# Kernel optimization log

Hardware: AMD Instinct MI355X
Metric: run time of the kernel (lower is better)

The kernel has to match this reference:

```python
import jax, jax.numpy as jnp
import numpy as np

T, H, I = 8192, 2048, 768  # tokens, hidden_size, intermediate_size

def setup_inputs() -> dict:
    key = jax.random.key(0)
    k1, k2, k3, k4 = jax.random.split(key, 4)
    x = jax.random.normal(k1, (T, H), dtype=jnp.float32)
    # torch nn.Linear weight layout: [out_features, in_features]
    gate_w = jax.random.normal(k2, (I, H), dtype=jnp.float32) * (1.0 / np.sqrt(H))
    up_w = jax.random.normal(k3, (I, H), dtype=jnp.float32) * (1.0 / np.sqrt(H))
    down_w = jax.random.normal(k4, (H, I), dtype=jnp.float32) * (1.0 / np.sqrt(I))
    return {"x": x, "gate_w": gate_w, "up_w": up_w, "down_w": down_w}

def reference(x, gate_w, up_w, down_w):
    # fused SwiGLU MLP: down( silu(x @ gate^T) * (x @ up^T) )
    gate = jnp.einsum('th,ih->ti', x, gate_w)   # [T, I]
    up = jnp.einsum('th,ih->ti', x, up_w)       # [T, I]
    h = jax.nn.silu(gate) * up                   # [T, I]
    out = jnp.einsum('ti,hi->th', h, down_w)     # [T, H]
    return out
```

## Files before the change

kernel.cpp:

```cpp
#include <hip/hip_runtime.h>
#include <hip/hip_bf16.h>
#include <stdint.h>

#define T_DIM 8192
#define H_DIM 2048
#define I_DIM 768

typedef __bf16 bf16_t;
typedef bf16_t bf16x8 __attribute__((ext_vector_type(8)));
typedef bf16_t bf16x4 __attribute__((ext_vector_type(4)));
typedef float  f32x4  __attribute__((ext_vector_type(4)));

__device__ __forceinline__ void async_load16(const void* g, void* s) {
    __builtin_amdgcn_global_load_lds(
        (const __attribute__((address_space(1))) void*)g,
        (__attribute__((address_space(3))) void*)s, 16, 0, 0);
}

__global__ __launch_bounds__(256) void cvt_kernel(
    const float* __restrict__ X, const float* __restrict__ G,
    const float* __restrict__ U, const float* __restrict__ D,
    bf16_t* __restrict__ Xb, bf16_t* __restrict__ Gb,
    bf16_t* __restrict__ Ub, bf16_t* __restrict__ Db)
{
    const size_t N4X = (size_t)T_DIM * H_DIM / 4;
    const size_t N4W = (size_t)I_DIM * H_DIM / 4;
    const size_t total = N4X + 3 * N4W;
    for (size_t i = (size_t)blockIdx.x * blockDim.x + threadIdx.x; i < total;
         i += (size_t)gridDim.x * blockDim.x) {
        const float* s; bf16_t* d; size_t j = i;
        if (j < N4X) { s = X; d = Xb; }
        else {
            j -= N4X;
            if (j < N4W) { s = G; d = Gb; }
            else { j -= N4W;
                if (j < N4W) { s = U; d = Ub; }
                else { j -= N4W; s = D; d = Db; } }
        }
        float4 v = ((const float4*)s)[j];
        bf16x4 o;
        o[0] = (bf16_t)v.x; o[1] = (bf16_t)v.y; o[2] = (bf16_t)v.z; o[3] = (bf16_t)v.w;
        ((bf16x4*)d)[j] = o;
    }
}

__global__ __launch_bounds__(256) void gateup_kernel(
    const bf16_t* __restrict__ X,
    const bf16_t* __restrict__ Wg,
    const bf16_t* __restrict__ Wu,
    bf16_t* __restrict__ Hbuf)
{
    __shared__ __align__(16) bf16_t sA[128 * 32];
    __shared__ __align__(16) bf16_t sG[64 * 32];
    __shared__ __align__(16) bf16_t sU[64 * 32];

    const int tid   = threadIdx.x;
    const int lane  = tid & 63;
    const int wave  = tid >> 6;
    const int waveM = wave >> 1;
    const int waveN = wave & 1;
    const int quad  = lane >> 4;
    const int lrow  = lane & 15;

    const int blockM = blockIdx.x;
    const int blockN = blockIdx.y;

    f32x4 accG[4][2], accU[4][2];
#pragma unroll
    for (int i = 0; i < 4; i++)
#pragma unroll
        for (int j = 0; j < 2; j++) { accG[i][j] = (f32x4)(0.f); accU[i][j] = (f32x4)(0.f); }

    const int s0 = tid, s1 = tid + 256;
    const int rA0 = s0 >> 2, cA0 = (s0 & 3) * 8;
    const int rA1 = s1 >> 2, cA1 = (s1 & 3) * 8;
    const int rW  = tid >> 2, cW  = (tid & 3) * 8;

    const bf16_t* Ab = X  + (size_t)(blockM * 128) * H_DIM;
    const bf16_t* Gb = Wg + (size_t)(blockN * 64) * H_DIM;
    const bf16_t* Ub = Wu + (size_t)(blockN * 64) * H_DIM;

    for (int k0 = 0; k0 < H_DIM; k0 += 32) {
        async_load16(Ab + (size_t)rA0 * H_DIM + k0 + cA0, &sA[s0 * 8]);
        async_load16(Ab + (size_t)rA1 * H_DIM + k0 + cA1, &sA[s1 * 8]);
        async_load16(Gb + (size_t)rW  * H_DIM + k0 + cW,  &sG[tid * 8]);
        async_load16(Ub + (size_t)rW  * H_DIM + k0 + cW,  &sU[tid * 8]);
        __syncthreads();

        bf16x8 aF[4], gF[2], uF[2];
#pragma unroll
        for (int mi = 0; mi < 4; mi++) {
            int r = waveM * 64 + mi * 16 + lrow;
            aF[mi] = *(const bf16x8*)&sA[r * 32 + quad * 8];
        }
#pragma unroll
        for (int ni = 0; ni < 2; ni++) {
            int r = waveN * 32 + ni * 16 + lrow;
            gF[ni] = *(const bf16x8*)&sG[r * 32 + quad * 8];
            uF[ni] = *(const bf16x8*)&sU[r * 32 + quad * 8];
        }
        __syncthreads();

#pragma unroll
        for (int mi = 0; mi < 4; mi++)
#pragma unroll
            for (int ni = 0; ni < 2; ni++) {
                accG[mi][ni] = __builtin_amdgcn_mfma_f32_16x16x32_bf16(aF[mi], gF[ni], accG[mi][ni], 0, 0, 0);
                accU[mi][ni] = __builtin_amdgcn_mfma_f32_16x16x32_bf16(aF[mi], uF[ni], accU[mi][ni], 0, 0, 0);
            }
    }

#pragma unroll
    for (int mi = 0; mi < 4; mi++) {
#pragma unroll
        for (int ni = 0; ni < 2; ni++) {
#pragma unroll
            for (int r = 0; r < 4; r++) {
                int row = blockM * 128 + waveM * 64 + mi * 16 + quad * 4 + r;
                int col = blockN * 64 + waveN * 32 + ni * 16 + lrow;
                float g = accG[mi][ni][r];
                float u = accU[mi][ni][r];
                float h = (g / (1.f + __expf(-g))) * u;
                Hbuf[(size_t)row * I_DIM + col] = (bf16_t)h;
            }
        }
    }
}

__global__ __launch_bounds__(256) void down_kernel(
    const bf16_t* __restrict__ Hbuf,
    const bf16_t* __restrict__ Wd,
    float* __restrict__ Out)
{
    __shared__ __align__(16) bf16_t sA[128 * 32];
    __shared__ __align__(16) bf16_t sB[128 * 32];

    const int tid   = threadIdx.x;
    const int lane  = tid & 63;
    const int wave  = tid >> 6;
    const int waveM = wave >> 1;
    const int waveN = wave & 1;
    const int quad  = lane >> 4;
    const int lrow  = lane & 15;

    const int blockM = blockIdx.x;
    const int blockN = blockIdx.y;

    f32x4 acc[4][4];
#pragma unroll
    for (int i = 0; i < 4; i++)
#pragma unroll
        for (int j = 0; j < 4; j++) acc[i][j] = (f32x4)(0.f);

    const int s0 = tid, s1 = tid + 256;
    const int rA0 = s0 >> 2, cA0 = (s0 & 3) * 8;
    const int rA1 = s1 >> 2, cA1 = (s1 & 3) * 8;

    const bf16_t* Ab = Hbuf + (size_t)(blockM * 128) * I_DIM;
    const bf16_t* Bb = Wd   + (size_t)(blockN * 128) * I_DIM;

    for (int k0 = 0; k0 < I_DIM; k0 += 32) {
        async_load16(Ab + (size_t)rA0 * I_DIM + k0 + cA0, &sA[s0 * 8]);
        async_load16(Ab + (size_t)rA1 * I_DIM + k0 + cA1, &sA[s1 * 8]);
        async_load16(Bb + (size_t)rA0 * I_DIM + k0 + cA0, &sB[s0 * 8]);
        async_load16(Bb + (size_t)rA1 * I_DIM + k0 + cA1, &sB[s1 * 8]);
        __syncthreads();

        bf16x8 aF[4], bF[4];
#pragma unroll
        for (int mi = 0; mi < 4; mi++) {
            int r = waveM * 64 + mi * 16 + lrow;
            aF[mi] = *(const bf16x8*)&sA[r * 32 + quad * 8];
        }
#pragma unroll
        for (int ni = 0; ni < 4; ni++) {
            int r = waveN * 64 + ni * 16 + lrow;
            bF[ni] = *(const bf16x8*)&sB[r * 32 + quad * 8];
        }
        __syncthreads();

#pragma unroll
        for (int mi = 0; mi < 4; mi++)
#pragma unroll
            for (int ni = 0; ni < 4; ni++)
                acc[mi][ni] = __builtin_amdgcn_mfma_f32_16x16x32_bf16(aF[mi], bF[ni], acc[mi][ni], 0, 0, 0);
    }

#pragma unroll
    for (int mi = 0; mi < 4; mi++) {
#pragma unroll
        for (int ni = 0; ni < 4; ni++) {
#pragma unroll
            for (int r = 0; r < 4; r++) {
                int row = blockM * 128 + waveM * 64 + mi * 16 + quad * 4 + r;
                int col = blockN * 128 + waveN * 64 + ni * 16 + lrow;
                Out[(size_t)row * H_DIM + col] = acc[mi][ni][r];
            }
        }
    }
}

extern "C" void kernel_launch(void* const* d_in, const int* in_sizes, int n_in,
                              void* d_out, int out_size, void* d_ws, size_t ws_size,
                              hipStream_t stream) {
    const float* x  = (const float*)d_in[0];
    const float* gw = (const float*)d_in[1];
    const float* uw = (const float*)d_in[2];
    const float* dw = (const float*)d_in[3];
    float* out = (float*)d_out;

    bf16_t* xb = (bf16_t*)d_ws;
    bf16_t* gb = xb + (size_t)T_DIM * H_DIM;
    bf16_t* ub = gb + (size_t)I_DIM * H_DIM;
    bf16_t* db = ub + (size_t)I_DIM * H_DIM;
    bf16_t* hb = db + (size_t)I_DIM * H_DIM;

    cvt_kernel<<<2048, 256, 0, stream>>>(x, gw, uw, dw, xb, gb, ub, db);
    gateup_kernel<<<dim3(T_DIM / 128, I_DIM / 64), 256, 0, stream>>>(xb, gb, ub, hb);
    down_kernel<<<dim3(T_DIM / 128, H_DIM / 128), 256, 0, stream>>>(hb, db, out);
}
```

Baseline: 229.2 us.

## Fuse activation bf16 conversion into gate/up GEMM and shrink down-proj tile

Stops converting x to bf16 in a separate pass. The gate/up kernel now loads fp32 x directly, converts it in registers and writes it to shared memory, while the weights keep using async LDS loads. The weight-only conversion kernel uses 8-wide vectors with one element group per thread. The down-projection N tile shrinks from 128 to 64, doubling the grid. This removes a full read and write of x through a bf16 copy, but x loads become synchronous register loads per K step, and every block re-converts its tile of x.

```diff
diff --git a/kernel.cpp b/kernel.cpp
--- a/kernel.cpp
+++ b/kernel.cpp
@@ -8,7 +8,6 @@
 
 typedef __bf16 bf16_t;
 typedef bf16_t bf16x8 __attribute__((ext_vector_type(8)));
-typedef bf16_t bf16x4 __attribute__((ext_vector_type(4)));
 typedef float  f32x4  __attribute__((ext_vector_type(4)));
 
 __device__ __forceinline__ void async_load16(const void* g, void* s) {
@@ -17,35 +16,27 @@
         (__attribute__((address_space(3))) void*)s, 16, 0, 0);
 }
 
-__global__ __launch_bounds__(256) void cvt_kernel(
-    const float* __restrict__ X, const float* __restrict__ G,
-    const float* __restrict__ U, const float* __restrict__ D,
-    bf16_t* __restrict__ Xb, bf16_t* __restrict__ Gb,
-    bf16_t* __restrict__ Ub, bf16_t* __restrict__ Db)
+__global__ __launch_bounds__(256) void cvt_w_kernel(
+    const float* __restrict__ G, const float* __restrict__ U,
+    const float* __restrict__ D,
+    bf16_t* __restrict__ Gb, bf16_t* __restrict__ Ub, bf16_t* __restrict__ Db)
 {
-    const size_t N4X = (size_t)T_DIM * H_DIM / 4;
-    const size_t N4W = (size_t)I_DIM * H_DIM / 4;
-    const size_t total = N4X + 3 * N4W;
-    for (size_t i = (size_t)blockIdx.x * blockDim.x + threadIdx.x; i < total;
-         i += (size_t)gridDim.x * blockDim.x) {
-        const float* s; bf16_t* d; size_t j = i;
-        if (j < N4X) { s = X; d = Xb; }
-        else {
-            j -= N4X;
-            if (j < N4W) { s = G; d = Gb; }
-            else { j -= N4W;
-                if (j < N4W) { s = U; d = Ub; }
-                else { j -= N4W; s = D; d = Db; } }
-        }
-        float4 v = ((const float4*)s)[j];
-        bf16x4 o;
-        o[0] = (bf16_t)v.x; o[1] = (bf16_t)v.y; o[2] = (bf16_t)v.z; o[3] = (bf16_t)v.w;
-        ((bf16x4*)d)[j] = o;
-    }
+    const size_t NG = (size_t)I_DIM * H_DIM / 8;
+    size_t g = (size_t)blockIdx.x * 256 + threadIdx.x;
+    const float* s; bf16_t* d;
+    if (g < NG)          { s = G; d = Gb; }
+    else if (g < 2 * NG) { s = U; d = Ub; g -= NG; }
+    else                 { s = D; d = Db; g -= 2 * NG; }
+    float4 v0 = ((const float4*)s)[2 * g];
+    float4 v1 = ((const float4*)s)[2 * g + 1];
+    bf16x8 o;
+    o[0] = (bf16_t)v0.x; o[1] = (bf16_t)v0.y; o[2] = (bf16_t)v0.z; o[3] = (bf16_t)v0.w;
+    o[4] = (bf16_t)v1.x; o[5] = (bf16_t)v1.y; o[6] = (bf16_t)v1.z; o[7] = (bf16_t)v1.w;
+    ((bf16x8*)d)[g] = o;
 }
 
 __global__ __launch_bounds__(256) void gateup_kernel(
-    const bf16_t* __restrict__ X,
+    const float*  __restrict__ X,
     const bf16_t* __restrict__ Wg,
     const bf16_t* __restrict__ Wu,
     bf16_t* __restrict__ Hbuf)
@@ -76,15 +67,26 @@
     const int rA1 = s1 >> 2, cA1 = (s1 & 3) * 8;
     const int rW  = tid >> 2, cW  = (tid & 3) * 8;
 
-    const bf16_t* Ab = X  + (size_t)(blockM * 128) * H_DIM;
+    const float*  Ab = X  + (size_t)(blockM * 128) * H_DIM;
     const bf16_t* Gb = Wg + (size_t)(blockN * 64) * H_DIM;
     const bf16_t* Ub = Wu + (size_t)(blockN * 64) * H_DIM;
 
     for (int k0 = 0; k0 < H_DIM; k0 += 32) {
-        async_load16(Ab + (size_t)rA0 * H_DIM + k0 + cA0, &sA[s0 * 8]);
-        async_load16(Ab + (size_t)rA1 * H_DIM + k0 + cA1, &sA[s1 * 8]);
-        async_load16(Gb + (size_t)rW  * H_DIM + k0 + cW,  &sG[tid * 8]);
-        async_load16(Ub + (size_t)rW  * H_DIM + k0 + cW,  &sU[tid * 8]);
+        async_load16(Gb + (size_t)rW * H_DIM + k0 + cW, &sG[tid * 8]);
+        async_load16(Ub + (size_t)rW * H_DIM + k0 + cW, &sU[tid * 8]);
+
+        const float* p0 = Ab + (size_t)rA0 * H_DIM + k0 + cA0;
+        const float* p1 = Ab + (size_t)rA1 * H_DIM + k0 + cA1;
+        f32x4 a00 = *(const f32x4*)p0, a01 = *(const f32x4*)(p0 + 4);
+        f32x4 a10 = *(const f32x4*)p1, a11 = *(const f32x4*)(p1 + 4);
+        bf16x8 w0, w1;
+#pragma unroll
+        for (int i = 0; i < 4; i++) {
+            w0[i] = (bf16_t)a00[i]; w0[4 + i] = (bf16_t)a01[i];
+            w1[i] = (bf16_t)a10[i]; w1[4 + i] = (bf16_t)a11[i];
+        }
+        *(bf16x8*)&sA[s0 * 8] = w0;
+        *(bf16x8*)&sA[s1 * 8] = w1;
         __syncthreads();
 
         bf16x8 aF[4], gF[2], uF[2];
@@ -133,7 +135,7 @@
     float* __restrict__ Out)
 {
     __shared__ __align__(16) bf16_t sA[128 * 32];
-    __shared__ __align__(16) bf16_t sB[128 * 32];
+    __shared__ __align__(16) bf16_t sB[64 * 32];
 
     const int tid   = threadIdx.x;
     const int lane  = tid & 63;
@@ -146,35 +148,35 @@
     const int blockM = blockIdx.x;
     const int blockN = blockIdx.y;
 
-    f32x4 acc[4][4];
+    f32x4 acc[4][2];
 #pragma unroll
     for (int i = 0; i < 4; i++)
 #pragma unroll
-        for (int j = 0; j < 4; j++) acc[i][j] = (f32x4)(0.f);
+        for (int j = 0; j < 2; j++) acc[i][j] = (f32x4)(0.f);
 
     const int s0 = tid, s1 = tid + 256;
     const int rA0 = s0 >> 2, cA0 = (s0 & 3) * 8;
     const int rA1 = s1 >> 2, cA1 = (s1 & 3) * 8;
+    const int rW  = tid >> 2, cW  = (tid & 3) * 8;
 
     const bf16_t* Ab = Hbuf + (size_t)(blockM * 128) * I_DIM;
-    const bf16_t* Bb = Wd   + (size_t)(blockN * 128) * I_DIM;
+    const bf16_t* Bb = Wd   + (size_t)(blockN * 64) * I_DIM;
 
     for (int k0 = 0; k0 < I_DIM; k0 += 32) {
         async_load16(Ab + (size_t)rA0 * I_DIM + k0 + cA0, &sA[s0 * 8]);
         async_load16(Ab + (size_t)rA1 * I_DIM + k0 + cA1, &sA[s1 * 8]);
-        async_load16(Bb + (size_t)rA0 * I_DIM + k0 + cA0, &sB[s0 * 8]);
-        async_load16(Bb + (size_t)rA1 * I_DIM + k0 + cA1, &sB[s1 * 8]);
-        __syncthreads();
-
-        bf16x8 aF[4], bF[4];
+        async_load16(Bb + (size_t)rW  * I_DIM + k0 + cW,  &sB[tid * 8]);
+        __syncthreads();
+
+        bf16x8 aF[4], bF[2];
 #pragma unroll
         for (int mi = 0; mi < 4; mi++) {
             int r = waveM * 64 + mi * 16 + lrow;
             aF[mi] = *(const bf16x8*)&sA[r * 32 + quad * 8];
         }
 #pragma unroll
-        for (int ni = 0; ni < 4; ni++) {
-            int r = waveN * 64 + ni * 16 + lrow;
+        for (int ni = 0; ni < 2; ni++) {
+            int r = waveN * 32 + ni * 16 + lrow;
             bF[ni] = *(const bf16x8*)&sB[r * 32 + quad * 8];
         }
         __syncthreads();
@@ -182,18 +184,18 @@
 #pragma unroll
         for (int mi = 0; mi < 4; mi++)
 #pragma unroll
-            for (int ni = 0; ni < 4; ni++)
+            for (int ni = 0; ni < 2; ni++)
                 acc[mi][ni] = __builtin_amdgcn_mfma_f32_16x16x32_bf16(aF[mi], bF[ni], acc[mi][ni], 0, 0, 0);
     }
 
 #pragma unroll
     for (int mi = 0; mi < 4; mi++) {
 #pragma unroll
-        for (int ni = 0; ni < 4; ni++) {
+        for (int ni = 0; ni < 2; ni++) {
 #pragma unroll
             for (int r = 0; r < 4; r++) {
                 int row = blockM * 128 + waveM * 64 + mi * 16 + quad * 4 + r;
-                int col = blockN * 128 + waveN * 64 + ni * 16 + lrow;
+                int col = blockN * 64 + waveN * 32 + ni * 16 + lrow;
                 Out[(size_t)row * H_DIM + col] = acc[mi][ni][r];
             }
         }
@@ -209,13 +211,13 @@
     const float* dw = (const float*)d_in[3];
     float* out = (float*)d_out;
 
-    bf16_t* xb = (bf16_t*)d_ws;
-    bf16_t* gb = xb + (size_t)T_DIM * H_DIM;
+    bf16_t* gb = (bf16_t*)d_ws;
     bf16_t* ub = gb + (size_t)I_DIM * H_DIM;
     bf16_t* db = ub + (size_t)I_DIM * H_DIM;
     bf16_t* hb = db + (size_t)I_DIM * H_DIM;
 
-    cvt_kernel<<<2048, 256, 0, stream>>>(x, gw, uw, dw, xb, gb, ub, db);
-    gateup_kernel<<<dim3(T_DIM / 128, I_DIM / 64), 256, 0, stream>>>(xb, gb, ub, hb);
-    down_kernel<<<dim3(T_DIM / 128, H_DIM / 128), 256, 0, stream>>>(hb, db, out);
-}
+    const int cvt_blocks = (int)(3 * (size_t)I_DIM * H_DIM / 8 / 256);
+    cvt_w_kernel<<<cvt_blocks, 256, 0, stream>>>(gw, uw, dw, gb, ub, db);
+    gateup_kernel<<<dim3(T_DIM / 128, I_DIM / 64), 256, 0, stream>>>(x, gb, ub, hb);
+    down_kernel<<<dim3(T_DIM / 128, H_DIM / 64), 256, 0, stream>>>(hb, db, out);
+}
```

After: 233.6 us. No clear change (+2.0%).
